# Kernel tuning notes

Hardware: AMD Instinct MI355X
Metric: run time of the kernel (lower is better)

Reference implementation:

```python
import jax, jax.numpy as jnp
import numpy as np

V, E, U, B, T = 50000, 128, 256, 256, 1024


def _lstm_cell(x, h, c, W, R, b):
    # Keras LSTMCell gate order: i, f, g(candidate), o
    z = x @ W + h @ R + b  # [B, 4U]
    i, f, g, o = jnp.split(z, 4, axis=-1)
    i = jax.nn.sigmoid(i)
    f = jax.nn.sigmoid(f)
    g = jnp.tanh(g)
    o = jax.nn.sigmoid(o)
    c_new = f * c + i * g
    h_new = o * jnp.tanh(c_new)
    return h_new, c_new


def setup_inputs() -> dict:
    key = jax.random.key(0)
    ks = jax.random.split(key, 10)
    s = lambda k, shape, scale: jax.random.normal(k, shape, dtype=jnp.float32) * scale
    return {
        "tokens": jax.random.randint(ks[0], (B, T), 0, V),
        "emb": s(ks[1], (V, E), 0.05),
        "W0": s(ks[2], (E, 4 * U), 1.0 / np.sqrt(E)),
        "R0": s(ks[3], (U, 4 * U), 1.0 / np.sqrt(U)),
        "b0": jnp.zeros((4 * U,), jnp.float32),
        "W1": s(ks[4], (U, 4 * U), 1.0 / np.sqrt(U)),
        "R1": s(ks[5], (U, 4 * U), 1.0 / np.sqrt(U)),
        "b1": jnp.zeros((4 * U,), jnp.float32),
        "Wout": s(ks[6], (U, 1), 1.0 / np.sqrt(U)),
        "bout": jnp.zeros((1,), jnp.float32),
    }


def reference(tokens, emb, W0, R0, b0, W1, R1, b1, Wout, bout):
    x = emb[tokens]                      # [B, T, E]
    xs = jnp.transpose(x, (1, 0, 2))     # [T, B, E] scan over time
    h0 = jnp.zeros((B, U), x.dtype)
    c0 = jnp.zeros((B, U), x.dtype)
    h1 = jnp.zeros((B, U), x.dtype)
    c1 = jnp.zeros((B, U), x.dtype)

    def step(carry, x_t):
        h0, c0, h1, c1 = carry
        h0, c0 = _lstm_cell(x_t, h0, c0, W0, R0, b0)
        h1, c1 = _lstm_cell(h0, h1, c1, W1, R1, b1)
        return (h0, c0, h1, c1), None

    (h0, c0, h1, c1), _ = jax.lax.scan(step, (h0, c0, h1, c1), xs)
    logits = h1 @ Wout + bout            # [B, 1]
    return jax.nn.sigmoid(logits)
```

## Files before the change

### kernel.cpp

```cpp
#include <hip/hip_runtime.h>

typedef unsigned short u16;
typedef unsigned int u32;
typedef unsigned long long u64;
typedef __attribute__((ext_vector_type(8))) short bf16x8;
typedef __attribute__((ext_vector_type(4))) float f32x4;

#define T_STEPS 1024
#define E_SZ 128
#define U_SZ 256

#define NG 16
#define MB 16
#define NSL 8
#define RD 8
#define HS 264
#define EPAD 136
#define BSTRIDE 192

#define POLL_BAIL 60000

#define L0_W0T 0
#define L0_R0T 34816
#define L0_X   102400
#define L0_G   106752
#define L0_STG 115520
#define L0_B   123712
#define L1_W1T 0
#define L1_R1T 67584
#define L1_SG0 135168
#define L1_SG1 143360
#define L1_G   151552
#define L1_B   160320
#define SMEM_TOTAL 160832

__device__ u64 g_exH0[RD * NG * NSL * BSTRIDE];
__device__ u64 g_exH1[2 * NG * NSL * BSTRIDE];
__device__ int g_pr[NG * NSL * 16];
__device__ u32 g_run;
__device__ int g_isF32;

__device__ __forceinline__ float bf2f(u16 u) {
  union { u32 i; float f; } v; v.i = ((u32)u) << 16; return v.f;
}
__device__ __forceinline__ u16 f2bf(float f) {
  union { u32 i; float f; } v; v.f = f;
  u32 r = v.i + 0x7fffu + ((v.i >> 16) & 1u);
  return (u16)(r >> 16);
}
__device__ __forceinline__ float sig_(float x) { return 1.f / (1.f + __expf(-x)); }
__device__ __forceinline__ float tnh_(float x) { return 2.f / (1.f + __expf(-2.f * x)) - 1.f; }

extern "C" __global__ void dtype_probe(const void* W0v) {
  __shared__ int cntBig;
  if (threadIdx.x == 0) cntBig = 0;
  __syncthreads();
  const u16* u = (const u16*)W0v;
  int big = 0;
  for (int i = threadIdx.x; i < 4096; i += 256)
    if ((u[i] & 0x7F80u) >= 0x4100u) big++;
  atomicAdd(&cntBig, big);
  __syncthreads();
  for (int i = threadIdx.x; i < NG * NSL * 16; i += 256) g_pr[i] = 0;
  if (threadIdx.x == 0) {
    g_isF32 = (cntBig > 100) ? 1 : 0;
    g_run = g_run + 1;
  }
}

__device__ __forceinline__ u64 ldAtom(const u64* p) {
  return __hip_atomic_load(p, __ATOMIC_RELAXED, __HIP_MEMORY_SCOPE_AGENT);
}

__device__ __forceinline__ int wavePollMin(const int* fA, int tgt, int lane,
                                           int& dead) {
  if (dead) return tgt;
  const int* p = (lane < 8) ? fA + lane * 16 : nullptr;
  int ok = (p == nullptr);
  int v = 0x7fffffff;
  int it = 0;
  while (!__all(ok)) {
    if (!ok) {
      v = __hip_atomic_load(p, __ATOMIC_RELAXED, __HIP_MEMORY_SCOPE_AGENT);
      ok = v >= tgt;
    }
    if (++it > POLL_BAIL) { dead = 1; break; }
    if (it > 48) __builtin_amdgcn_s_sleep(1);
  }
  __atomic_signal_fence(__ATOMIC_ACQUIRE);
  int m = (lane < 8) ? v : 0x7fffffff;
#pragma unroll
  for (int off = 4; off; off >>= 1) {
    int o = __shfl_down(m, off);
    m = m < o ? m : o;
  }
  return __shfl(m, 0);
}

__device__ __forceinline__ void unpackToLds(const u64 q0, const u64 q1, const u64 q2,
                                            u16* __restrict__ stg, int slice,
                                            int ml, int quad) {
  u32 a0 = (u32)q0, a1 = (u32)(q0 >> 32);
  u32 b0 = (u32)q1, b1 = (u32)(q1 >> 32);
  u32 c0 = (u32)q2;
  uint4 F;
  F.x = a0;
  F.y = (a1 & 0xFFFFu) | (b0 << 16);
  F.z = (b0 >> 16) | (b1 << 16);
  F.w = c0;
  *(uint4*)(stg + (((slice << 4) + ml) * 4 + quad) * 8) = F;
}

__device__ __forceinline__ void stageOne(const u64* __restrict__ base, u32 etag,
                                         u16* __restrict__ stg,
                                         int wv, int ml, int quad, int& dead) {
  const int j0 = wv << 1;
  const u64* p0 = base + (u64)j0 * BSTRIDE + ml * 12 + quad * 3;
  const u64* p1 = p0 + BSTRIDE;
  u64 qa0 = ldAtom(p0), qa1 = ldAtom(p0 + 1), qa2 = ldAtom(p0 + 2);
  u64 qb0 = ldAtom(p1), qb1 = ldAtom(p1 + 1), qb2 = ldAtom(p1 + 2);
  int it = 0;
  while (true) {
    u32 badA = (((u32)(qa0 >> 48)) ^ etag) | (((u32)(qa1 >> 48)) ^ etag) |
               (((u32)(qa2 >> 48)) ^ etag);
    u32 badB = (((u32)(qb0 >> 48)) ^ etag) | (((u32)(qb1 >> 48)) ^ etag) |
               (((u32)(qb2 >> 48)) ^ etag);
    if (!__any((badA | badB) != 0)) break;
    if (dead) break;
    if (++it > POLL_BAIL) { dead = 1; break; }
    if (badA) { qa0 = ldAtom(p0); qa1 = ldAtom(p0 + 1); qa2 = ldAtom(p0 + 2); }
    if (badB) { qb0 = ldAtom(p1); qb1 = ldAtom(p1 + 1); qb2 = ldAtom(p1 + 2); }
    if (it > 8) __builtin_amdgcn_s_sleep(1);
  }
  __atomic_signal_fence(__ATOMIC_ACQUIRE);
  unpackToLds(qa0, qa1, qa2, stg, j0, ml, quad);
  unpackToLds(qb0, qb1, qb2, stg, j0 + 1, ml, quad);
}

__device__ __forceinline__ void stageDual(const u64* __restrict__ b0, u32 e0,
                                          u16* __restrict__ s0,
                                          const u64* __restrict__ b1, u32 e1,
                                          u16* __restrict__ s1, int doH1,
                                          int wv, int ml, int quad, int& dead) {
  const int j0 = wv << 1;
  const int off = ml * 12 + quad * 3;
  const u64* p0a = b0 + (u64)j0 * BSTRIDE + off;
  const u64* p0b = p0a + BSTRIDE;
  const u64* p1a = b1 + (u64)j0 * BSTRIDE + off;
  const u64* p1b = p1a + BSTRIDE;
  u64 xa0 = ldAtom(p0a), xa1 = ldAtom(p0a + 1), xa2 = ldAtom(p0a + 2);
  u64 xb0 = ldAtom(p0b), xb1 = ldAtom(p0b + 1), xb2 = ldAtom(p0b + 2);
  u64 ya0 = 0, ya1 = 0, ya2 = 0, yb0 = 0, yb1 = 0, yb2 = 0;
  if (doH1) {
    ya0 = ldAtom(p1a); ya1 = ldAtom(p1a + 1); ya2 = ldAtom(p1a + 2);
    yb0 = ldAtom(p1b); yb1 = ldAtom(p1b + 1); yb2 = ldAtom(p1b + 2);
  }
  int it = 0;
  while (true) {
    u32 badA = (((u32)(xa0 >> 48)) ^ e0) | (((u32)(xa1 >> 48)) ^ e0) |
               (((u32)(xa2 >> 48)) ^ e0);
    u32 badB = (((u32)(xb0 >> 48)) ^ e0) | (((u32)(xb1 >> 48)) ^ e0) |
               (((u32)(xb2 >> 48)) ^ e0);
    u32 badC = 0, badD = 0;
    if (doH1) {
      badC = (((u32)(ya0 >> 48)) ^ e1) | (((u32)(ya1 >> 48)) ^ e1) |
             (((u32)(ya2 >> 48)) ^ e1);
      badD = (((u32)(yb0 >> 48)) ^ e1) | (((u32)(yb1 >> 48)) ^ e1) |
             (((u32)(yb2 >> 48)) ^ e1);
    }
    if (!__any((badA | badB | badC | badD) != 0)) break;
    if (dead) break;
    if (++it > POLL_BAIL) { dead = 1; break; }
    if (badA) { xa0 = ldAtom(p0a); xa1 = ldAtom(p0a + 1); xa2 = ldAtom(p0a + 2); }
    if (badB) { xb0 = ldAtom(p0b); xb1 = ldAtom(p0b + 1); xb2 = ldAtom(p0b + 2); }
    if (badC) { ya0 = ldAtom(p1a); ya1 = ldAtom(p1a + 1); ya2 = ldAtom(p1a + 2); }
    if (badD) { yb0 = ldAtom(p1b); yb1 = ldAtom(p1b + 1); yb2 = ldAtom(p1b + 2); }
    if (it > 8) __builtin_amdgcn_s_sleep(1);
  }
  __atomic_signal_fence(__ATOMIC_ACQUIRE);
  unpackToLds(xa0, xa1, xa2, s0, j0, ml, quad);
  unpackToLds(xb0, xb1, xb2, s0, j0 + 1, ml, quad);
  if (doH1) {
    unpackToLds(ya0, ya1, ya2, s1, j0, ml, quad);
    unpackToLds(yb0, yb1, yb2, s1, j0 + 1, ml, quad);
  }
}

extern "C" __global__ void __launch_bounds__(256, 1)
lstm_fused(const int* __restrict__ tokens, const void* __restrict__ emb,
           const void* __restrict__ W0, const void* __restrict__ R0, const void* __restrict__ b0,
           const void* __restrict__ W1, const void* __restrict__ R1, const void* __restrict__ b1,
           const void* __restrict__ Wout, const void* __restrict__ bout,
           void* __restrict__ outv) {
  extern __shared__ char smem[];

  const int tid = threadIdx.x;
  const int b = blockIdx.x;
  const int g = b & (NG - 1);
  const int w = b >> 4;
  const int role = w >> 3;
  const int sl = w & 7;
  const int isF32 = g_isF32;
  const u32 tagB = ((u32)g_run) << 10;

  auto ldf = [&](const void* p, int idx) -> float {
    return isF32 ? ((const float*)p)[idx] : bf2f(((const u16*)p)[idx]);
  };

  const int lane = tid & 63;
  const int wv = tid >> 6;
  const int ml = lane & 15;
  const int quad = lane >> 4;
  const int um = tid >> 4;
  const int un = tid & 15;

  const int mB = tid >> 4;
  const int uS = tid & 15;
  const int qS = uS / 3;
  const int sS = uS - qS * 3;
  const int kb = (qS << 3) + 3 * sS;
  const int nFull = (sS != 2);

  int* flp = g_pr + (g << 3) * 16;
  int dead = 0;

  if (role == 0) {
    u16* w0t = (u16*)(smem + L0_W0T);
    u16* r0t = (u16*)(smem + L0_R0T);
    u16* ldsX = (u16*)(smem + L0_X);
    float* ldsG = (float*)(smem + L0_G);
    u16* stg = (u16*)(smem + L0_STG);
    float* ldsB = (float*)(smem + L0_B);

    for (int i = tid; i < 128 * 128; i += 256) {
      int k = i >> 7, n = i & 127;
      int col = ((n >> 5) << 8) + (sl << 5) + (n & 31);
      w0t[n * EPAD + k] = f2bf(ldf(W0, k * 1024 + col));
    }
    for (int i = tid; i < 128 * 256; i += 256) {
      int k = i >> 7, n = i & 127;
      int col = ((n >> 5) << 8) + (sl << 5) + (n & 31);
      r0t[n * HS + k] = f2bf(ldf(R0, k * 1024 + col));
    }
    if (tid < 128) {
      int col = ((tid >> 5) << 8) + (sl << 5) + (tid & 31);
      ldsB[tid] = ldf(b0, col);
    }

    float cst[3] = {0.f, 0.f, 0.f};
    const int tokBase = (g * MB + um) * T_STEPS;
    int prMin = 0;

    float4 xfA, xfB; uint4 xbf;
    {
      int tok = tokens[tokBase];
      if (isF32) {
        const float* row = (const float*)emb + (u64)tok * E_SZ + (un << 3);
        xfA = *(const float4*)row; xfB = *(const float4*)(row + 4);
      } else {
        xbf = *(const uint4*)((const u16*)emb + (u64)tok * E_SZ + (un << 3));
      }
    }
    __syncthreads();

    const int row0 = (wv << 5) + ml;
    const u16* brA0 = w0t + row0 * EPAD + (quad << 3);
    const u16* brB0 = brA0 + (EPAD << 4);
    const u16* brA2 = r0t + row0 * HS + (quad << 3);
    const u16* brB2 = brA2 + (HS << 4);

    for (int t = 0; t < T_STEPS; t++) {
      if (t >= RD && prMin < t - RD + 1)
        prMin = wavePollMin(flp, t - RD + 1, lane, dead);

      {
        uint4 pk;
        if (isF32) {
          pk.x = (u32)f2bf(xfA.x) | ((u32)f2bf(xfA.y) << 16);
          pk.y = (u32)f2bf(xfA.z) | ((u32)f2bf(xfA.w) << 16);
          pk.z = (u32)f2bf(xfB.x) | ((u32)f2bf(xfB.y) << 16);
          pk.w = (u32)f2bf(xfB.z) | ((u32)f2bf(xfB.w) << 16);
        } else pk = xbf;
        *(uint4*)(ldsX + um * EPAD + (un << 3)) = pk;
      }
      __syncthreads();

      float ba = ldsB[row0], bb = ldsB[row0 + 16];
      f32x4 acA = {ba, ba, ba, ba}, acB = {bb, bb, bb, bb};

      {
        const u16* ar = ldsX + ml * EPAD + (quad << 3);
#pragma unroll
        for (int kc = 0; kc < 4; kc++) {
          bf16x8 av = *(const bf16x8*)(ar + kc * 32);
          acA = __builtin_amdgcn_mfma_f32_16x16x32_bf16(av, *(const bf16x8*)(brA0 + kc * 32), acA, 0, 0, 0);
          acB = __builtin_amdgcn_mfma_f32_16x16x32_bf16(av, *(const bf16x8*)(brB0 + kc * 32), acB, 0, 0, 0);
        }
      }

      if (t > 0) {
        const u64* base = g_exH0 +
            (u64)((((t - 1) & (RD - 1)) * NG + g) * NSL) * BSTRIDE;
        stageOne(base, (tagB + t) & 0xFFFFu, stg, wv, ml, quad, dead);
        __syncthreads();
#pragma unroll
        for (int j = 0; j < NSL; j++) {
          bf16x8 fv = *(const bf16x8*)(stg + (((j << 4) + ml) * 4 + quad) * 8);
          acA = __builtin_amdgcn_mfma_f32_16x16x32_bf16(fv, *(const bf16x8*)(brA2 + (j << 5)), acA, 0, 0, 0);
          acB = __builtin_amdgcn_mfma_f32_16x16x32_bf16(fv, *(const bf16x8*)(brB2 + (j << 5)), acB, 0, 0, 0);
        }
      }

#pragma unroll
      for (int r = 0; r < 4; r++) {
        int m = (quad << 2) + r;
        float gA = (wv == 2) ? tnh_(acA[r]) : sig_(acA[r]);
        float gB = (wv == 2) ? tnh_(acB[r]) : sig_(acB[r]);
        ldsG[row0 * 17 + m] = gA;
        ldsG[(row0 + 16) * 17 + m] = gB;
      }
      __syncthreads();

      if (uS < 12) {
        u64 val = ((u64)((tagB + t + 1) & 0xFFFFu)) << 48;
#pragma unroll
        for (int i2 = 0; i2 < 3; i2++) {
          if (i2 < 2 || nFull) {
            int k = kb + i2;
            float iv = ldsG[k * 17 + mB];
            float fv = ldsG[(32 + k) * 17 + mB];
            float gv = ldsG[(64 + k) * 17 + mB];
            float ov = ldsG[(96 + k) * 17 + mB];
            float c = fv * cst[i2] + iv * gv; cst[i2] = c;
            val |= ((u64)f2bf(ov * tnh_(c))) << (16 * i2);
          }
        }
        u64 elem = (u64)(((t & (RD - 1)) * NG + g) * NSL + sl) * BSTRIDE +
                   mB * 12 + uS;
        __hip_atomic_store(g_exH0 + elem, val,
                           __ATOMIC_RELAXED, __HIP_MEMORY_SCOPE_AGENT);
      }

      if (t + 1 < T_STEPS) {
        int tok = tokens[tokBase + t + 1];
        if (isF32) {
          const float* row = (const float*)emb + (u64)tok * E_SZ + (un << 3);
          xfA = *(const float4*)row; xfB = *(const float4*)(row + 4);
        } else {
          xbf = *(const uint4*)((const u16*)emb + (u64)tok * E_SZ + (un << 3));
        }
      }
    }
  } else {
    u16* w1t = (u16*)(smem + L1_W1T);
    u16* r1t = (u16*)(smem + L1_R1T);
    u16* stg0 = (u16*)(smem + L1_SG0);
    u16* stg1 = (u16*)(smem + L1_SG1);
    float* ldsG = (float*)(smem + L1_G);
    float* ldsB = (float*)(smem + L1_B);

    for (int i = tid; i < 128 * 256; i += 256) {
      int k = i >> 7, n = i & 127;
      int col = ((n >> 5) << 8) + (sl << 5) + (n & 31);
      w1t[n * HS + k] = f2bf(ldf(W1, k * 1024 + col));
      r1t[n * HS + k] = f2bf(ldf(R1, k * 1024 + col));
    }
    if (tid < 128) {
      int col = ((tid >> 5) << 8) + (sl << 5) + (tid & 31);
      ldsB[tid] = ldf(b1, col);
    }
    __syncthreads();

    float cst[3] = {0.f, 0.f, 0.f};
    const int row0 = (wv << 5) + ml;
    const u16* brA1 = w1t + row0 * HS + (quad << 3);
    const u16* brB1 = brA1 + (HS << 4);
    const u16* brA2 = r1t + row0 * HS + (quad << 3);
    const u16* brB2 = brA2 + (HS << 4);

    for (int t = 0; t < T_STEPS; t++) {
      {
        const u64* h0base = g_exH0 +
            (u64)(((t & (RD - 1)) * NG + g) * NSL) * BSTRIDE;
        const u64* h1base = g_exH1 +
            (u64)((((t - 1) & 1) * NG + g) * NSL) * BSTRIDE;
        stageDual(h0base, (tagB + t + 1) & 0xFFFFu, stg0,
                  h1base, (tagB + t) & 0xFFFFu, stg1, (t > 0),
                  wv, ml, quad, dead);
      }
      __syncthreads();

      if (tid == 0) {
        __atomic_signal_fence(__ATOMIC_RELEASE);
        __hip_atomic_store(g_pr + ((g << 3) + sl) * 16, t + 1,
                           __ATOMIC_RELAXED, __HIP_MEMORY_SCOPE_AGENT);
      }

      float ba = ldsB[row0], bb = ldsB[row0 + 16];
      f32x4 acA = {ba, ba, ba, ba}, acB = {bb, bb, bb, bb};

#pragma unroll
      for (int j = 0; j < NSL; j++) {
        bf16x8 fv = *(const bf16x8*)(stg0 + (((j << 4) + ml) * 4 + quad) * 8);
        acA = __builtin_amdgcn_mfma_f32_16x16x32_bf16(fv, *(const bf16x8*)(brA1 + (j << 5)), acA, 0, 0, 0);
        acB = __builtin_amdgcn_mfma_f32_16x16x32_bf16(fv, *(const bf16x8*)(brB1 + (j << 5)), acB, 0, 0, 0);
      }
      if (t > 0) {
#pragma unroll
        for (int j = 0; j < NSL; j++) {
          bf16x8 fv = *(const bf16x8*)(stg1 + (((j << 4) + ml) * 4 + quad) * 8);
          acA = __builtin_amdgcn_mfma_f32_16x16x32_bf16(fv, *(const bf16x8*)(brA2 + (j << 5)), acA, 0, 0, 0);
          acB = __builtin_amdgcn_mfma_f32_16x16x32_bf16(fv, *(const bf16x8*)(brB2 + (j << 5)), acB, 0, 0, 0);
        }
      }

#pragma unroll
      for (int r = 0; r < 4; r++) {
        int m = (quad << 2) + r;
        float gA = (wv == 2) ? tnh_(acA[r]) : sig_(acA[r]);
        float gB = (wv == 2) ? tnh_(acB[r]) : sig_(acB[r]);
        ldsG[row0 * 17 + m] = gA;
        ldsG[(row0 + 16) * 17 + m] = gB;
      }
      __syncthreads();

      if (uS < 12) {
        u64 val = ((u64)((tagB + t + 1) & 0xFFFFu)) << 48;
#pragma unroll
        for (int i2 = 0; i2 < 3; i2++) {
          if (i2 < 2 || nFull) {
            int k = kb + i2;
            float iv = ldsG[k * 17 + mB];
            float fv = ldsG[(32 + k) * 17 + mB];
            float gv = ldsG[(64 + k) * 17 + mB];
            float ov = ldsG[(96 + k) * 17 + mB];
            float c = fv * cst[i2] + iv * gv; cst[i2] = c;
            val |= ((u64)f2bf(ov * tnh_(c))) << (16 * i2);
          }
        }
        u64 elem = (u64)(((t & 1) * NG + g) * NSL + sl) * BSTRIDE +
                   mB * 12 + uS;
        __hip_atomic_store(g_exH1 + elem, val,
                           __ATOMIC_RELAXED, __HIP_MEMORY_SCOPE_AGENT);
      }
      __syncthreads();
    }

    if (sl == 0) {
      u16* ldsEpi = stg0;
      const u32 etag = (tagB + T_STEPS) & 0xFFFFu;
      if (uS < 12) {
        for (int sp = 0; sp < 8; sp++) {
          const u64* p = g_exH1 +
              (u64)(((1) * NG + g) * NSL + sp) * BSTRIDE + mB * 12 + uS;
          u64 v; int it = 0;
          while (true) {
            v = ldAtom(p);
            if ((u32)(v >> 48) == etag) break;
            if (dead) break;
            if (++it > POLL_BAIL) { dead = 1; break; }
            if (it > 8) __builtin_amdgcn_s_sleep(1);
          }
          u16* dst = ldsEpi + mB * HS + (sp << 5) + kb;
          dst[0] = (u16)v;
          dst[1] = (u16)(v >> 16);
          if (nFull) dst[2] = (u16)(v >> 32);
        }
      }
      __syncthreads();
      float* woutf = ldsG;
      float* red = ldsG + 272;
      woutf[tid] = ldf(Wout, tid);
      __syncthreads();
      float p = 0.f;
#pragma unroll
      for (int j = 0; j < 16; j++)
        p += bf2f(ldsEpi[um * HS + (un << 4) + j]) * woutf[(un << 4) + j];
      red[um * 17 + un] = p;
      __syncthreads();
      if (tid < 16) {
        float sum = ldf(bout, 0);
#pragma unroll
        for (int j = 0; j < 16; j++) sum += red[tid * 17 + j];
        float val = sig_(sum);
        if (isF32) ((float*)outv)[g * MB + tid] = val;
        else       ((u16*)outv)[g * MB + tid] = f2bf(val);
      }
    }
  }
}

extern "C" void kernel_launch(void* const* d_in, const int* in_sizes, int n_in,
                              void* d_out, int out_size, void* d_ws, size_t ws_size,
                              hipStream_t stream) {
  const int* tokens = (const int*)d_in[0];
  const void* emb  = d_in[1];
  const void* W0   = d_in[2];
  const void* R0   = d_in[3];
  const void* b0   = d_in[4];
  const void* W1   = d_in[5];
  const void* R1   = d_in[6];
  const void* b1   = d_in[7];
  const void* Wout = d_in[8];
  const void* bout = d_in[9];

  hipFuncSetAttribute((const void*)lstm_fused,
                      hipFuncAttributeMaxDynamicSharedMemorySize, SMEM_TOTAL);

  dtype_probe<<<dim3(1), dim3(256), 0, stream>>>(W0);

  lstm_fused<<<dim3(256), dim3(256), SMEM_TOTAL, stream>>>(
      tokens, emb, W0, R0, b0, W1, R1, b1, Wout, bout, d_out);
}
```

Baseline: 3.133 ms.

## Interleave gate columns so LSTM cell update runs in registers via shuffles

```diff
diff --git a/kernel.cpp b/kernel.cpp
--- a/kernel.cpp
+++ b/kernel.cpp
@@ -23,16 +23,15 @@
 #define L0_W0T 0
 #define L0_R0T 34816
 #define L0_X   102400
-#define L0_G   106752
-#define L0_STG 115520
-#define L0_B   123712
+#define L0_STG 106752
+#define L0_B   114944
 #define L1_W1T 0
 #define L1_R1T 67584
 #define L1_SG0 135168
 #define L1_SG1 143360
-#define L1_G   151552
-#define L1_B   160320
-#define SMEM_TOTAL 160832
+#define L1_B   151552
+#define L1_EPIF 152064
+#define SMEM_TOTAL 154624
 
 __device__ u64 g_exH0[RD * NG * NSL * BSTRIDE];
 __device__ u64 g_exH1[2 * NG * NSL * BSTRIDE];
@@ -186,6 +185,60 @@
   }
 }
 
+__device__ __forceinline__ void gateCellPost(f32x4 acA, f32x4 acB,
+                                             float* cstA, float* cstB,
+                                             int lane, int wv, u32 etag,
+                                             u64* __restrict__ exch, u64 blk) {
+  const int ml = lane & 15;
+  const int gg = ml & 3;
+  const int isT = (gg == 2);
+  u32 hpack = 0;
+#pragma unroll
+  for (int r = 0; r < 4; r++) {
+    float vA = isT ? tnh_(acA[r]) : sig_(acA[r]);
+    float vB = isT ? tnh_(acB[r]) : sig_(acB[r]);
+    float vA1 = __shfl_xor(vA, 1), vA2 = __shfl_xor(vA, 2);
+    float vA3 = __shfl_xor(vA2, 1);
+    float vB1 = __shfl_xor(vB, 1), vB2 = __shfl_xor(vB, 2);
+    float vB3 = __shfl_xor(vB2, 1);
+    float iA = gg == 0 ? vA : (gg == 1 ? vA1 : (gg == 2 ? vA2 : vA3));
+    float fA = gg == 1 ? vA : (gg == 0 ? vA1 : (gg == 3 ? vA2 : vA3));
+    float gA = gg == 2 ? vA : (gg == 3 ? vA1 : (gg == 0 ? vA2 : vA3));
+    float oA = gg == 3 ? vA : (gg == 2 ? vA1 : (gg == 1 ? vA2 : vA3));
+    float iB = gg == 0 ? vB : (gg == 1 ? vB1 : (gg == 2 ? vB2 : vB3));
+    float fB = gg == 1 ? vB : (gg == 0 ? vB1 : (gg == 3 ? vB2 : vB3));
+    float gB = gg == 2 ? vB : (gg == 3 ? vB1 : (gg == 0 ? vB2 : vB3));
+    float oB = gg == 3 ? vB : (gg == 2 ? vB1 : (gg == 1 ? vB2 : vB3));
+    float cA = fA * cstA[r] + iA * gA; cstA[r] = cA;
+    float cB = fB * cstB[r] + iB * gB; cstB[r] = cB;
+    float hA = oA * tnh_(cA);
+    float hB = oB * tnh_(cB);
+    u32 pk = (u32)f2bf(hA) | ((u32)f2bf(hB) << 16);
+    hpack = (r == gg) ? pk : hpack;
+  }
+  const int m_ = lane & 15, db = lane >> 4;
+  u32 w0, w1, w2;
+  {
+    int jp0 = 3 * db, jp1 = jp0 + 1, jp2 = jp0 + 2;
+    int sb = ((m_ >> 2) << 4) + (m_ & 3);
+    u32 t0 = (u32)__builtin_amdgcn_ds_bpermute((sb + ((jp0 & 3) << 2)) << 2, (int)hpack);
+    u32 t1 = (u32)__builtin_amdgcn_ds_bpermute((sb + ((jp1 & 3) << 2)) << 2, (int)hpack);
+    u32 t2 = (u32)__builtin_amdgcn_ds_bpermute((sb + ((jp2 & 3) << 2)) << 2, (int)hpack);
+    w0 = (jp0 & 4) ? (t0 >> 16) : (t0 & 0xFFFFu);
+    w1 = (jp1 & 4) ? (t1 >> 16) : (t1 & 0xFFFFu);
+    w2 = (jp2 & 4) ? (t2 >> 16) : (t2 & 0xFFFFu);
+  }
+  if (db < 3) {
+    u64 val = ((u64)etag) << 48;
+    val |= (u64)w0;
+    val |= ((u64)w1) << 16;
+    if (db != 2) val |= ((u64)w2) << 32;
+    u64 elem = blk * BSTRIDE + (u64)(m_ * 12 + wv * 3 + db);
+    __hip_atomic_store(exch + elem, val,
+                       __ATOMIC_RELAXED, __HIP_MEMORY_SCOPE_AGENT);
+  }
+}
+
 extern "C" __global__ void __launch_bounds__(256, 1)
 lstm_fused(const int* __restrict__ tokens, const void* __restrict__ emb,
            const void* __restrict__ W0, const void* __restrict__ R0, const void* __restrict__ b0,
@@ -214,12 +267,9 @@
   const int um = tid >> 4;
   const int un = tid & 15;
 
-  const int mB = tid >> 4;
-  const int uS = tid & 15;
-  const int qS = uS / 3;
-  const int sS = uS - qS * 3;
-  const int kb = (qS << 3) + 3 * sS;
-  const int nFull = (sS != 2);
+  auto colg = [&](int n) -> int {
+    return ((n & 3) << 8) + (sl << 5) + (n >> 2);
+  };
 
   int* flp = g_pr + (g << 3) * 16;
   int dead = 0;
@@ -228,26 +278,21 @@
     u16* w0t = (u16*)(smem + L0_W0T);
     u16* r0t = (u16*)(smem + L0_R0T);
     u16* ldsX = (u16*)(smem + L0_X);
-    float* ldsG = (float*)(smem + L0_G);
     u16* stg = (u16*)(smem + L0_STG);
     float* ldsB = (float*)(smem + L0_B);
 
     for (int i = tid; i < 128 * 128; i += 256) {
       int k = i >> 7, n = i & 127;
-      int col = ((n >> 5) << 8) + (sl << 5) + (n & 31);
-      w0t[n * EPAD + k] = f2bf(ldf(W0, k * 1024 + col));
+      w0t[n * EPAD + k] = f2bf(ldf(W0, k * 1024 + colg(n)));
     }
     for (int i = tid; i < 128 * 256; i += 256) {
       int k = i >> 7, n = i & 127;
-      int col = ((n >> 5) << 8) + (sl << 5) + (n & 31);
-      r0t[n * HS + k] = f2bf(ldf(R0, k * 1024 + col));
-    }
-    if (tid < 128) {
-      int col = ((tid >> 5) << 8) + (sl << 5) + (tid & 31);
-      ldsB[tid] = ldf(b0, col);
-    }
-
-    float cst[3] = {0.f, 0.f, 0.f};
+      r0t[n * HS + k] = f2bf(ldf(R0, k * 1024 + colg(n)));
+    }
+    if (tid < 128) ldsB[tid] = ldf(b0, colg(tid));
+
+    float cstA[4] = {0.f, 0.f, 0.f, 0.f};
+    float cstB[4] = {0.f, 0.f, 0.f, 0.f};
     const int tokBase = (g * MB + um) * T_STEPS;
     int prMin = 0;
 
@@ -302,7 +347,10 @@
         const u64* base = g_exH0 +
             (u64)((((t - 1) & (RD - 1)) * NG + g) * NSL) * BSTRIDE;
         stageOne(base, (tagB + t) & 0xFFFFu, stg, wv, ml, quad, dead);
-        __syncthreads();
+      }
+      __syncthreads();
+
+      if (t > 0) {
 #pragma unroll
         for (int j = 0; j < NSL; j++) {
           bf16x8 fv = *(const bf16x8*)(stg + (((j << 4) + ml) * 4 + quad) * 8);
@@ -311,35 +359,8 @@
         }
       }
 
-#pragma unroll
-      for (int r = 0; r < 4; r++) {
-        int m = (quad << 2) + r;
-        float gA = (wv == 2) ? tnh_(acA[r]) : sig_(acA[r]);
-        float gB = (wv == 2) ? tnh_(acB[r]) : sig_(acB[r]);
-        ldsG[row0 * 17 + m] = gA;
-        ldsG[(row0 + 16) * 17 + m] = gB;
-      }
-      __syncthreads();
-
-      if (uS < 12) {
-        u64 val = ((u64)((tagB + t + 1) & 0xFFFFu)) << 48;
-#pragma unroll
-        for (int i2 = 0; i2 < 3; i2++) {
-          if (i2 < 2 || nFull) {
-            int k = kb + i2;
-            float iv = ldsG[k * 17 + mB];
-            float fv = ldsG[(32 + k) * 17 + mB];
-            float gv = ldsG[(64 + k) * 17 + mB];
-            float ov = ldsG[(96 + k) * 17 + mB];
-            float c = fv * cst[i2] + iv * gv; cst[i2] = c;
-            val |= ((u64)f2bf(ov * tnh_(c))) << (16 * i2);
-          }
-        }
-        u64 elem = (u64)(((t & (RD - 1)) * NG + g) * NSL + sl) * BSTRIDE +
-                   mB * 12 + uS;
-        __hip_atomic_store(g_exH0 + elem, val,
-                           __ATOMIC_RELAXED, __HIP_MEMORY_SCOPE_AGENT);
-      }
+      gateCellPost(acA, acB, cstA, cstB, lane, wv, (tagB + t + 1) & 0xFFFFu,
+                   g_exH0, (u64)(((t & (RD - 1)) * NG + g) * NSL + sl));
 
       if (t + 1 < T_STEPS) {
         int tok = tokens[tokBase + t + 1];
@@ -356,22 +377,18 @@
     u16* r1t = (u16*)(smem + L1_R1T);
     u16* stg0 = (u16*)(smem + L1_SG0);
     u16* stg1 = (u16*)(smem + L1_SG1);
-    float* ldsG = (float*)(smem + L1_G);
     float* ldsB = (float*)(smem + L1_B);
 
     for (int i = tid; i < 128 * 256; i += 256) {
       int k = i >> 7, n = i & 127;
-      int col = ((n >> 5) << 8) + (sl << 5) + (n & 31);
-      w1t[n * HS + k] = f2bf(ldf(W1, k * 1024 + col));
-      r1t[n * HS + k] = f2bf(ldf(R1, k * 1024 + col));
-    }
-    if (tid < 128) {
-      int col = ((tid >> 5) << 8) + (sl << 5) + (tid & 31);
-      ldsB[tid] = ldf(b1, col);
-    }
+      w1t[n * HS + k] = f2bf(ldf(W1, k * 1024 + colg(n)));
+      r1t[n * HS + k] = f2bf(ldf(R1, k * 1024 + colg(n)));
+    }
+    if (tid < 128) ldsB[tid] = ldf(b1, colg(tid));
     __syncthreads();
 
-    float cst[3] = {0.f, 0.f, 0.f};
+    float cstA[4] = {0.f, 0.f, 0.f, 0.f};
+    float cstB[4] = {0.f, 0.f, 0.f, 0.f};
     const int row0 = (wv << 5) + ml;
     const u16* brA1 = w1t + row0 * HS + (quad << 3);
     const u16* brB1 = brA1 + (HS << 4);
@@ -414,41 +431,23 @@
         }
       }
 
-#pragma unroll
-      for (int r = 0; r < 4; r++) {
-        int m = (quad << 2) + r;
-        float gA = (wv == 2) ? tnh_(acA[r]) : sig_(acA[r]);
-        float gB = (wv == 2) ? tnh_(acB[r]) : sig_(acB[r]);
-        ldsG[row0 * 17 + m] = gA;
-        ldsG[(row0 + 16) * 17 + m] = gB;
-      }
-      __syncthreads();
-
-      if (uS < 12) {
-        u64 val = ((u64)((tagB + t + 1) & 0xFFFFu)) << 48;
-#pragma unroll
-        for (int i2 = 0; i2 < 3; i2++) {
-          if (i2 < 2 || nFull) {
-            int k = kb + i2;
-            float iv = ldsG[k * 17 + mB];
-            float fv = ldsG[(32 + k) * 17 + mB];
-            float gv = ldsG[(64 + k) * 17 + mB];
-            float ov = ldsG[(96 + k) * 17 + mB];
-            float c = fv * cst[i2] + iv * gv; cst[i2] = c;
-            val |= ((u64)f2bf(ov * tnh_(c))) << (16 * i2);
-          }
-        }
-        u64 elem = (u64)(((t & 1) * NG + g) * NSL + sl) * BSTRIDE +
-                   mB * 12 + uS;
-        __hip_atomic_store(g_exH1 + elem, val,
-                           __ATOMIC_RELAXED, __HIP_MEMORY_SCOPE_AGENT);
-      }
+      gateCellPost(acA, acB, cstA, cstB, lane, wv, (tagB + t + 1) & 0xFFFFu,
+                   g_exH1, (u64)(((t & 1) * NG + g) * NSL + sl));
+
       __syncthreads();
     }
 
     if (sl == 0) {
       u16* ldsEpi = stg0;
+      float* woutf = (float*)(smem + L1_EPIF);
+      float* red = woutf + 272;
       const u32 etag = (tagB + T_STEPS) & 0xFFFFu;
+      const int mB = tid >> 4;
+      const int uS = tid & 15;
+      const int qS = uS / 3;
+      const int sS = uS - qS * 3;
+      const int kb = (qS << 3) + 3 * sS;
+      const int nFull = (sS != 2);
       if (uS < 12) {
         for (int sp = 0; sp < 8; sp++) {
           const u64* p = g_exH1 +
@@ -468,8 +467,6 @@
         }
       }
       __syncthreads();
-      float* woutf = ldsG;
-      float* red = ldsG + 272;
       woutf[tid] = ldf(Wout, tid);
       __syncthreads();
       float p = 0.f;
```

After: 3.907 ms. +24.7%, slower.
